# Kernel tuning notes

Hardware: AMD Instinct MI355X
Metric: run time of the kernel (lower is better)

The kernel has to match this reference:

```python
import jax, jax.numpy as jnp
import numpy as np


def _ln(x, g, b, eps=1e-5):
    m = x.mean(-1, keepdims=True)
    v = ((x - m) ** 2).mean(-1, keepdims=True)
    return (x - m) * jax.lax.rsqrt(v + eps) * g + b


def setup_inputs() -> dict:
    key = jax.random.key(0)
    ks = jax.random.split(key, 16)
    B, C, D, H, W = 1, 192, 8, 32, 32
    nh, k, hid = 6, 7, 768
    n = lambda i, shape: jax.random.normal(ks[i], shape, dtype=jnp.float32) * 0.02
    return {
        'x': jax.random.normal(ks[0], (B, C, D, H, W), dtype=jnp.float32),
        'pos_emb': n(1, (1, D, C)),
        't_ln1_g': jnp.ones((C,), jnp.float32), 't_ln1_b': jnp.zeros((C,), jnp.float32),
        't_qkv_w': n(2, (C, 3 * C)),
        't_out_w': n(3, (C, C)), 't_out_b': jnp.zeros((C,), jnp.float32),
        't_ln2_g': jnp.ones((C,), jnp.float32), 't_ln2_b': jnp.zeros((C,), jnp.float32),
        't_fc1_w': n(4, (C, hid)), 't_fc1_b': jnp.zeros((hid,), jnp.float32),
        't_fc2_w': n(5, (hid, C)), 't_fc2_b': jnp.zeros((C,), jnp.float32),
        't_lnf_g': jnp.ones((C,), jnp.float32), 't_lnf_b': jnp.zeros((C,), jnp.float32),
        's_ln1_g': jnp.ones((C,), jnp.float32), 's_ln1_b': jnp.zeros((C,), jnp.float32),
        's_qkv_w': n(6, (C, 3 * C)), 's_qkv_b': jnp.zeros((3 * C,), jnp.float32),
        's_rpb': n(7, (nh, 2 * k - 1, 2 * k - 1)),
        's_proj_w': n(8, (C, C)), 's_proj_b': jnp.zeros((C,), jnp.float32),
        's_ln2_g': jnp.ones((C,), jnp.float32), 's_ln2_b': jnp.zeros((C,), jnp.float32),
        's_fc1_w': n(9, (C, hid)), 's_fc1_b': jnp.zeros((hid,), jnp.float32),
        's_fc2_w': n(10, (hid, C)), 's_fc2_b': jnp.zeros((C,), jnp.float32),
    }


def reference(x, pos_emb, t_ln1_g, t_ln1_b, t_qkv_w, t_out_w, t_out_b,
              t_ln2_g, t_ln2_b, t_fc1_w, t_fc1_b, t_fc2_w, t_fc2_b,
              t_lnf_g, t_lnf_b, s_ln1_g, s_ln1_b, s_qkv_w, s_qkv_b, s_rpb,
              s_proj_w, s_proj_b, s_ln2_g, s_ln2_b, s_fc1_w, s_fc1_b,
              s_fc2_w, s_fc2_b):
    B, C, D, H, W = x.shape
    nh = 6
    d = C // nh
    k = 7
    scale = d ** -0.5

    # ---- Time transformer: attend over the D frames per spatial position ----
    t = jnp.transpose(x, (0, 3, 4, 2, 1)).reshape(B * H * W, D, C)  # (b h w) s c
    t = t + pos_emb
    y = _ln(t, t_ln1_g, t_ln1_b)
    qkv = (y @ t_qkv_w).reshape(-1, D, 3, nh, d)
    q, kk, v = [jnp.transpose(qkv[:, :, i], (0, 2, 1, 3)) for i in range(3)]  # [N,nh,D,d]
    att = jax.nn.softmax(jnp.einsum('nhid,nhjd->nhij', q, kk) * scale, axis=-1)
    o = jnp.einsum('nhij,nhjd->nhid', att, v)
    o = jnp.transpose(o, (0, 2, 1, 3)).reshape(-1, D, C)
    t = t + (o @ t_out_w + t_out_b)
    y = _ln(t, t_ln2_g, t_ln2_b)
    t = t + (jax.nn.gelu(y @ t_fc1_w + t_fc1_b, approximate=False) @ t_fc2_w + t_fc2_b)
    t = _ln(t, t_lnf_g, t_lnf_b)
    x = x + jnp.transpose(t.reshape(B, H, W, D, C), (0, 4, 3, 1, 2))

    # ---- Space transformer: neighborhood (NAT) attention per frame ----
    s = jnp.transpose(x, (0, 2, 3, 4, 1)).reshape(B * D, H, W, C)  # (b s) h w c
    shortcut = s
    y = _ln(s, s_ln1_g, s_ln1_b)
    qkv = (y @ s_qkv_w + s_qkv_b).reshape(B * D, H, W, 3, nh, d)
    qkv = jnp.transpose(qkv, (3, 0, 4, 1, 2, 5))  # [3,N,nh,H,W,d]
    q, kk, v = qkv[0] * scale, qkv[1], qkv[2]
    half = k // 2
    sh = jnp.clip(jnp.arange(H) - half, 0, H - k)   # window start per row (edge-clamped)
    sw = jnp.clip(jnp.arange(W) - half, 0, W - k)
    idx_h = sh[:, None] + jnp.arange(k)             # [H,k] neighbor rows
    idx_w = sw[:, None] + jnp.arange(k)             # [W,k] neighbor cols
    rel_h = idx_h - jnp.arange(H)[:, None] + (k - 1)  # rel-pos-bias indices in [0,2k-2]
    rel_w = idx_w - jnp.arange(W)[:, None] + (k - 1)
    Kn = kk[:, :, idx_h][:, :, :, :, idx_w]  # [N,nh,H,k,W,k,d]
    Vn = v[:, :, idx_h][:, :, :, :, idx_w]
    att = jnp.einsum('nehwd,nehawbd->nehwab', q, Kn)  # [N,nh,H,W,k,k]
    bias = jnp.transpose(s_rpb[:, rel_h][:, :, :, rel_w], (0, 1, 3, 2, 4))  # [nh,H,W,k,k]
    att = att + bias[None]
    shp = att.shape
    att = jax.nn.softmax(att.reshape(shp[0], shp[1], shp[2], shp[3], k * k), axis=-1).reshape(shp)
    o = jnp.einsum('nehwab,nehawbd->nehwd', att, Vn)
    o = jnp.transpose(o, (0, 2, 3, 1, 4)).reshape(B * D, H, W, C)
    s = shortcut + (o @ s_proj_w + s_proj_b)
    y = _ln(s, s_ln2_g, s_ln2_b)
    s = s + (jax.nn.gelu(y @ s_fc1_w + s_fc1_b, approximate=False) @ s_fc2_w + s_fc2_b)
    x_space = jnp.transpose(s.reshape(B, D, H, W, C), (0, 4, 1, 2, 3))
    return x + x_space
```

## Files before the change

kernel.cpp:

```cpp
#include <hip/hip_runtime.h>
#include <hip/hip_bf16.h>
#include <math.h>

typedef __hip_bfloat16 bf16;
typedef short bf16x8 __attribute__((ext_vector_type(8)));
typedef float f32x4 __attribute__((ext_vector_type(4)));

__device__ __forceinline__ float b2f(bf16 v) { return __bfloat162float(v); }
__device__ __forceinline__ bf16 f2b(float v) { return __float2bfloat16(v); }
__device__ __forceinline__ float us2f(unsigned short u) {
  return __uint_as_float(((unsigned)u) << 16);
}
__device__ __forceinline__ unsigned short f2us(float f) {
  bf16 h = __float2bfloat16(f);
  return *reinterpret_cast<unsigned short*>(&h);
}
__device__ __forceinline__ float ldin(const void* p, size_t i, int f32) {
  return f32 ? ((const float*)p)[i] : b2f(((const bf16*)p)[i]);
}

#define CC 192
#define DD 8
#define HH 32
#define WW 32
#define NHEAD 6
#define HDIM 32
#define HID 768
#define NTOK 8192
#define ATT_SCALE 0.17677669529663687f

__global__ void wconv_kernel(const unsigned short* __restrict__ xu,
                             const void* w0, const void* w1, const void* w2,
                             const void* w3, const void* w4, const void* w5,
                             const void* w6, const void* w7,
                             bf16* __restrict__ WT, int* __restrict__ flag) {
  __shared__ int cnt[4];
  {
    float a = fabsf(us2f(xu[threadIdx.x]));
    bool insane = !((a == 0.0f) || (a > 9.5e-7f && a < 64.0f));
    unsigned long long mask = __ballot(insane);
    if ((threadIdx.x & 63) == 0) cnt[threadIdx.x >> 6] = __popcll(mask);
  }
  __syncthreads();
  int f32 = (cnt[0] + cnt[1] + cnt[2] + cnt[3]) > 32;
  if (blockIdx.x == 0 && threadIdx.x == 0) *flag = f32;

  int idx = blockIdx.x * 256 + threadIdx.x;
  if (idx >= 884736) return;
  const void* src; int K, N, loc;
  if      (idx < 110592) { src = w0; K = 192; N = 576; loc = idx; }
  else if (idx < 147456) { src = w1; K = 192; N = 192; loc = idx - 110592; }
  else if (idx < 294912) { src = w2; K = 192; N = 768; loc = idx - 147456; }
  else if (idx < 442368) { src = w3; K = 768; N = 192; loc = idx - 294912; }
  else if (idx < 552960) { src = w4; K = 192; N = 576; loc = idx - 442368; }
  else if (idx < 589824) { src = w5; K = 192; N = 192; loc = idx - 552960; }
  else if (idx < 737280) { src = w6; K = 192; N = 768; loc = idx - 589824; }
  else                   { src = w7; K = 768; N = 192; loc = idx - 737280; }
  int n = loc / K, k = loc - n * K;
  WT[idx] = f2b(ldin(src, (size_t)k * N + n, f32));
}

#define WOFF_TQKV  0
#define WOFF_TOUT  110592
#define WOFF_TFC1  147456
#define WOFF_TFC2  294912
#define WOFF_SQKV  442368
#define WOFF_SPROJ 552960
#define WOFF_SFC1  589824
#define WOFF_SFC2  737280

__global__ void build_ln1_kernel(const void* __restrict__ x, const void* __restrict__ pos,
                                 const void* __restrict__ g, const void* __restrict__ b,
                                 float* __restrict__ T, bf16* __restrict__ Y,
                                 const int* __restrict__ dfl) {
  int f32 = *dfl;
  int wave = (blockIdx.x * blockDim.x + threadIdx.x) >> 6;
  int lane = threadIdx.x & 63;
  if (wave >= NTOK) return;
  int d = wave & 7, hw = wave >> 3;
  float v[3];
#pragma unroll
  for (int e = 0; e < 3; e++) {
    int c = lane + e * 64;
    v[e] = ldin(x, (size_t)((c << 3) + d) * 1024 + hw, f32) +
           ldin(pos, (size_t)d * CC + c, f32);
  }
  float* tr = T + (size_t)wave * CC;
#pragma unroll
  for (int e = 0; e < 3; e++) tr[lane + e * 64] = v[e];
  float s = v[0] + v[1] + v[2];
  for (int off = 32; off; off >>= 1) s += __shfl_xor(s, off);
  float mean = s * (1.0f / CC);
  float d0 = v[0] - mean, d1 = v[1] - mean, d2 = v[2] - mean;
  float q = d0 * d0 + d1 * d1 + d2 * d2;
  for (int off = 32; off; off >>= 1) q += __shfl_xor(q, off);
  float rstd = rsqrtf(q * (1.0f / CC) + 1e-5f);
  bf16* o = Y + (size_t)wave * CC;
  o[lane]       = f2b(d0 * rstd * ldin(g, lane, f32)       + ldin(b, lane, f32));
  o[lane + 64]  = f2b(d1 * rstd * ldin(g, lane + 64, f32)  + ldin(b, lane + 64, f32));
  o[lane + 128] = f2b(d2 * rstd * ldin(g, lane + 128, f32) + ldin(b, lane + 128, f32));
}

__global__ void ln_kernel(const float* __restrict__ in, bf16* __restrict__ out,
                          const void* __restrict__ g, const void* __restrict__ b,
                          int rows, const int* __restrict__ dfl) {
  int f32 = *dfl;
  int wave = (blockIdx.x * blockDim.x + threadIdx.x) >> 6;
  int lane = threadIdx.x & 63;
  if (wave >= rows) return;
  const float* r = in + (size_t)wave * CC;
  float v0 = r[lane], v1 = r[lane + 64], v2 = r[lane + 128];
  float s = v0 + v1 + v2;
  for (int off = 32; off; off >>= 1) s += __shfl_xor(s, off);
  float mean = s * (1.0f / CC);
  float d0 = v0 - mean, d1 = v1 - mean, d2 = v2 - mean;
  float q = d0 * d0 + d1 * d1 + d2 * d2;
  for (int off = 32; off; off >>= 1) q += __shfl_xor(q, off);
  float rstd = rsqrtf(q * (1.0f / CC) + 1e-5f);
  bf16* o = out + (size_t)wave * CC;
  o[lane]       = f2b(d0 * rstd * ldin(g, lane, f32)       + ldin(b, lane, f32));
  o[lane + 64]  = f2b(d1 * rstd * ldin(g, lane + 64, f32)  + ldin(b, lane + 64, f32));
  o[lane + 128] = f2b(d2 * rstd * ldin(g, lane + 128, f32) + ldin(b, lane + 128, f32));
}

template <int TM, bool BIAS, bool GELU, bool RES, bool OUTBF, bool FINAL>
__global__ void gemm_kernel(const bf16* __restrict__ A, const bf16* __restrict__ WT,
                            const void* __restrict__ bias, const float* __restrict__ R,
                            void* __restrict__ Cout, const float* __restrict__ X2,
                            int M, int N, int K, const int* __restrict__ dfl) {
  int f32 = *dfl;
  __shared__ __align__(16) unsigned short As[TM * 64 * 72];
  __shared__ __align__(16) unsigned short Bs[64 * 72];
  int bm = blockIdx.y * (TM * 64), bn = blockIdx.x * 64;
  int tid = threadIdx.x;
  int w = tid >> 6;
  int lane = tid & 63;
  int lm = lane & 15;
  int lk = lane >> 4;

  f32x4 acc[TM][4];
#pragma unroll
  for (int i = 0; i < TM; i++)
#pragma unroll
    for (int j = 0; j < 4; j++) acc[i][j] = (f32x4){0.f, 0.f, 0.f, 0.f};

  const unsigned short* Au = reinterpret_cast<const unsigned short*>(A);
  const unsigned short* Wu = reinterpret_cast<const unsigned short*>(WT);

  for (int k0 = 0; k0 < K; k0 += 64) {
#pragma unroll
    for (int u = 0; u < TM * 2; u++) {
      int unit = tid + u * 256;
      int row = unit >> 3, seg = unit & 7;
      uint4 v = *reinterpret_cast<const uint4*>(
          &Au[(size_t)(bm + row) * K + k0 + seg * 8]);
      *reinterpret_cast<uint4*>(&As[row * 72 + seg * 8]) = v;
    }
#pragma unroll
    for (int u = 0; u < 2; u++) {
      int unit = tid + u * 256;
      int n = unit >> 3, seg = unit & 7;
      uint4 v = *reinterpret_cast<const uint4*>(
          &Wu[(size_t)(bn + n) * K + k0 + seg * 8]);
      *reinterpret_cast<uint4*>(&Bs[n * 72 + seg * 8]) = v;
    }
    __syncthreads();

#pragma unroll
    for (int kc = 0; kc < 2; kc++) {
      bf16x8 af[TM], bfr[4];
#pragma unroll
      for (int tm = 0; tm < TM; tm++)
        af[tm] = *reinterpret_cast<const bf16x8*>(
            &As[(w * (TM * 16) + tm * 16 + lm) * 72 + kc * 32 + lk * 8]);
#pragma unroll
      for (int tn = 0; tn < 4; tn++)
        bfr[tn] = *reinterpret_cast<const bf16x8*>(
            &Bs[(tn * 16 + lm) * 72 + kc * 32 + lk * 8]);
#pragma unroll
      for (int tm = 0; tm < TM; tm++)
#pragma unroll
        for (int tn = 0; tn < 4; tn++)
          acc[tm][tn] = __builtin_amdgcn_mfma_f32_16x16x32_bf16(
              af[tm], bfr[tn], acc[tm][tn], 0, 0, 0);
    }
    __syncthreads();
  }

#pragma unroll
  for (int tn = 0; tn < 4; tn++) {
    int col = bn + tn * 16 + lm;
    float bv = BIAS ? ldin(bias, col, f32) : 0.f;
#pragma unroll
    for (int tm = 0; tm < TM; tm++) {
      int row0 = bm + w * (TM * 16) + tm * 16 + lk * 4;
#pragma unroll
      for (int r = 0; r < 4; r++) {
        int row = row0 + r;
        float v = acc[tm][tn][r];
        if (BIAS) v += bv;
        if (GELU) v = 0.5f * v * (1.0f + erff(v * 0.70710678118654752f));
        size_t idx = (size_t)row * N + col;
        if (RES) v += R[idx];
        if (FINAL) {
          float o = v + X2[(size_t)row * CC + col];
          if (f32) ((float*)Cout)[(size_t)col * NTOK + row] = o;
          else     ((bf16*)Cout)[(size_t)col * NTOK + row] = f2b(o);
        } else if (OUTBF) {
          ((bf16*)Cout)[idx] = f2b(v);
        } else {
          ((float*)Cout)[idx] = v;
        }
      }
    }
  }
}

__global__ void time_attn_kernel(const bf16* __restrict__ qkv, bf16* __restrict__ O) {
  __shared__ float q[NHEAD][DD][HDIM];
  __shared__ float k[NHEAD][DD][HDIM];
  __shared__ float v[NHEAD][DD][HDIM];
  __shared__ float p[NHEAD][DD][DD];
  int n = blockIdx.x;
  int head = threadIdx.x >> 5;
  int dd = threadIdx.x & 31;
  for (int s = 0; s < DD; s++) {
    const bf16* row = qkv + (size_t)(n * DD + s) * (3 * CC);
    q[head][s][dd] = b2f(row[head * HDIM + dd]);
    k[head][s][dd] = b2f(row[CC + head * HDIM + dd]);
    v[head][s][dd] = b2f(row[2 * CC + head * HDIM + dd]);
  }
  __syncthreads();
  for (int pair = dd; pair < 64; pair += 32) {
    int sq = pair >> 3, sk = pair & 7;
    float sum = 0.f;
#pragma unroll
    for (int e = 0; e < HDIM; e++) sum += q[head][sq][e] * k[head][sk][e];
    p[head][sq][sk] = sum * ATT_SCALE;
  }
  __syncthreads();
  if (dd < DD) {
    float mx = -1e30f;
    for (int sk = 0; sk < DD; sk++) mx = fmaxf(mx, p[head][dd][sk]);
    float sum = 0.f;
    for (int sk = 0; sk < DD; sk++) { float e = expf(p[head][dd][sk] - mx); p[head][dd][sk] = e; sum += e; }
    float inv = 1.0f / sum;
    for (int sk = 0; sk < DD; sk++) p[head][dd][sk] *= inv;
  }
  __syncthreads();
  for (int sq = 0; sq < DD; sq++) {
    float sum = 0.f;
#pragma unroll
    for (int sk = 0; sk < DD; sk++) sum += p[head][sq][sk] * v[head][sk][dd];
    O[(size_t)(n * DD + sq) * CC + head * HDIM + dd] = f2b(sum);
  }
}

__global__ void epi_ln1_kernel(const float* __restrict__ T, const void* __restrict__ x,
                               const void* __restrict__ gf, const void* __restrict__ bf,
                               const void* __restrict__ g1, const void* __restrict__ b1,
                               float* __restrict__ X1T, bf16* __restrict__ Y,
                               const int* __restrict__ dfl) {
  int f32 = *dfl;
  int wave = (blockIdx.x * blockDim.x + threadIdx.x) >> 6;
  int lane = threadIdx.x & 63;
  if (wave >= NTOK) return;
  const float* r = T + (size_t)wave * CC;
  float v0 = r[lane], v1 = r[lane + 64], v2 = r[lane + 128];
  float s = v0 + v1 + v2;
  for (int off = 32; off; off >>= 1) s += __shfl_xor(s, off);
  float mean = s * (1.0f / CC);
  float d0 = v0 - mean, d1 = v1 - mean, d2 = v2 - mean;
  float q = d0 * d0 + d1 * d1 + d2 * d2;
  for (int off = 32; off; off >>= 1) q += __shfl_xor(q, off);
  float rstd = rsqrtf(q * (1.0f / CC) + 1e-5f);
  int d = wave & 7, hw = wave >> 3;
  int m = d * 1024 + hw;
  float xv[3];
#pragma unroll
  for (int e = 0; e < 3; e++) {
    int c = lane + e * 64;
    float dv = (e == 0 ? d0 : (e == 1 ? d1 : d2));
    float normed = dv * rstd * ldin(gf, c, f32) + ldin(bf, c, f32);
    xv[e] = ldin(x, (size_t)((c << 3) + d) * 1024 + hw, f32) + normed;
  }
  float* o = X1T + (size_t)m * CC;
#pragma unroll
  for (int e = 0; e < 3; e++) o[lane + e * 64] = xv[e];
  float s2 = xv[0] + xv[1] + xv[2];
  for (int off = 32; off; off >>= 1) s2 += __shfl_xor(s2, off);
  float mean2 = s2 * (1.0f / CC);
  float e0 = xv[0] - mean2, e1 = xv[1] - mean2, e2 = xv[2] - mean2;
  float q2 = e0 * e0 + e1 * e1 + e2 * e2;
  for (int off = 32; off; off >>= 1) q2 += __shfl_xor(q2, off);
  float rstd2 = rsqrtf(q2 * (1.0f / CC) + 1e-5f);
  bf16* y = Y + (size_t)m * CC;
  y[lane]       = f2b(e0 * rstd2 * ldin(g1, lane, f32)       + ldin(b1, lane, f32));
  y[lane + 64]  = f2b(e1 * rstd2 * ldin(g1, lane + 64, f32)  + ldin(b1, lane + 64, f32));
  y[lane + 128] = f2b(e2 * rstd2 * ldin(g1, lane + 128, f32) + ldin(b1, lane + 128, f32));
}

#define NKEY 224
#define PKS 40
#define PVS 232
__global__ void nat_attn_kernel(const bf16* __restrict__ qkv, const void* __restrict__ rpb,
                                bf16* __restrict__ O, const int* __restrict__ dfl) {
  int f32 = *dfl;
  __shared__ __align__(16) unsigned short Ks[NKEY * PKS];
  __shared__ __align__(16) unsigned short Vs[32 * PVS];
  __shared__ __align__(16) unsigned short Qs[64 * PKS];
  __shared__ __align__(16) unsigned short Ps[64 * PVS];
  __shared__ float rb[176];

  int blk = blockIdx.x;
  int frame = blk & 7;
  int rest = blk >> 3;
  int h = rest % 6;
  int tile = rest / 6;
  int ty = tile >> 2, tx = tile & 3;
  int base_h = min(max(ty * 8 - 3, 0), HH - 7);
  int base_w = min(max(tx * 8 - 3, 0), WW - 7);

  int tid = threadIdx.x;

  for (int i = tid; i < 169; i += 256) rb[i] = ldin(rpb, (size_t)h * 169 + i, f32);
  for (int u = tid; u < 784; u += 256) {
    int j = u >> 2, seg = u & 3;
    int a = j / 14, bb = j - a * 14;
    int ih = min(base_h + a, HH - 1), iw = min(base_w + bb, WW - 1);
    int mg = frame * 1024 + ih * 32 + iw;
    uint4 v = *reinterpret_cast<const uint4*>(qkv + (size_t)mg * 576 + 192 + h * 32 + seg * 8);
    *reinterpret_cast<uint4*>(&Ks[j * PKS + seg * 8]) = v;
  }
  for (int u = tid; u < 784; u += 256) {
    int j = u >> 2, seg = u & 3;
    int a = j / 14, bb = j - a * 14;
    int ih = min(base_h + a, HH - 1), iw = min(base_w + bb, WW - 1);
    int mg = frame * 1024 + ih * 32 + iw;
    uint4 v = *reinterpret_cast<const uint4*>(qkv + (size_t)mg * 576 + 384 + h * 32 + seg * 8);
    unsigned arr[4] = {v.x, v.y, v.z, v.w};
#pragma unroll
    for (int e = 0; e < 4; e++) {
      Vs[(seg * 8 + e * 2) * PVS + j]     = (unsigned short)(arr[e] & 0xffffu);
      Vs[(seg * 8 + e * 2 + 1) * PVS + j] = (unsigned short)(arr[e] >> 16);
    }
  }
  for (int u = tid; u < 32 * (PVS - 196); u += 256) {
    int dd = u / (PVS - 196), c = 196 + u % (PVS - 196);
    Vs[dd * PVS + c] = 0;
  }
  {
    int q = tid >> 2, seg = tid & 3;
    int qy = ty * 8 + (q >> 3), qx = tx * 8 + (q & 7);
    int mg = frame * 1024 + qy * 32 + qx;
    uint4 v = *reinterpret_cast<const uint4*>(qkv + (size_t)mg * 576 + h * 32 + seg * 8);
    *reinterpret_cast<uint4*>(&Qs[q * PKS + seg * 8]) = v;
  }
  __syncthreads();

  int w = tid >> 6;
  int lane = tid & 63;
  int c = lane & 15;
  int lk = lane >> 4;

  bf16x8 aq = *reinterpret_cast<const bf16x8*>(&Qs[(w * 16 + c) * PKS + lk * 8]);
  f32x4 sc[14];
#pragma unroll
  for (int f = 0; f < 14; f++) {
    bf16x8 bk = *reinterpret_cast<const bf16x8*>(&Ks[(f * 16 + c) * PKS + lk * 8]);
    sc[f] = __builtin_amdgcn_mfma_f32_16x16x32_bf16(aq, bk, (f32x4){0.f, 0.f, 0.f, 0.f}, 0, 0, 0);
  }

#pragma unroll
  for (int f = 0; f < 14; f++) {
    int key = f * 16 + c;
    int a = key / 14, bb = key - a * 14;
    int ih = base_h + a, iw = base_w + bb;
    bool keyok = key < 196;
#pragma unroll
    for (int r = 0; r < 4; r++) {
      int qloc = w * 16 + lk * 4 + r;
      int qy = ty * 8 + (qloc >> 3), qx = tx * 8 + (qloc & 7);
      int sh = min(max(qy - 3, 0), HH - 7);
      int sw = min(max(qx - 3, 0), WW - 7);
      bool valid = keyok && ((unsigned)(ih - sh) < 7u) && ((unsigned)(iw - sw) < 7u);
      int bidx = valid ? (ih - qy + 6) * 13 + (iw - qx + 6) : 0;
      float s = sc[f][r] * ATT_SCALE + rb[bidx];
      sc[f][r] = valid ? s : -1e30f;
    }
  }

  float sm[4];
#pragma unroll
  for (int r = 0; r < 4; r++) {
    float m = sc[0][r];
#pragma unroll
    for (int f = 1; f < 14; f++) m = fmaxf(m, sc[f][r]);
    for (int off = 8; off; off >>= 1) m = fmaxf(m, __shfl_xor(m, off));
    float s = 0.f;
#pragma unroll
    for (int f = 0; f < 14; f++) { float e = __expf(sc[f][r] - m); sc[f][r] = e; s += e; }
    for (int off = 8; off; off >>= 1) s += __shfl_xor(s, off);
    sm[r] = 1.0f / s;
  }
#pragma unroll
  for (int f = 0; f < 14; f++)
#pragma unroll
    for (int r = 0; r < 4; r++)
      Ps[(w * 16 + lk * 4 + r) * PVS + f * 16 + c] = f2us(sc[f][r] * sm[r]);
  __syncthreads();

  f32x4 oacc[2] = {(f32x4){0.f, 0.f, 0.f, 0.f}, (f32x4){0.f, 0.f, 0.f, 0.f}};
#pragma unroll
  for (int kt = 0; kt < 7; kt++) {
    bf16x8 ap = *reinterpret_cast<const bf16x8*>(&Ps[(w * 16 + c) * PVS + kt * 32 + lk * 8]);
#pragma unroll
    for (int dt = 0; dt < 2; dt++) {
      bf16x8 bv = *reinterpret_cast<const bf16x8*>(&Vs[(dt * 16 + c) * PVS + kt * 32 + lk * 8]);
      oacc[dt] = __builtin_amdgcn_mfma_f32_16x16x32_bf16(ap, bv, oacc[dt], 0, 0, 0);
    }
  }

#pragma unroll
  for (int dt = 0; dt < 2; dt++)
#pragma unroll
    for (int r = 0; r < 4; r++) {
      int qloc = w * 16 + lk * 4 + r;
      int qy = ty * 8 + (qloc >> 3), qx = tx * 8 + (qloc & 7);
      int mg = frame * 1024 + qy * 32 + qx;
      O[(size_t)mg * CC + h * 32 + dt * 16 + c] = f2b(oacc[dt][r]);
    }
}

extern "C" void kernel_launch(void* const* d_in, const int* in_sizes, int n_in,
                              void* d_out, int out_size, void* d_ws, size_t ws_size,
                              hipStream_t stream) {
  const void* x        = d_in[0];
  const void* pos_emb  = d_in[1];
  const void* t_ln1_g  = d_in[2];
  const void* t_ln1_b  = d_in[3];
  const void* t_qkv_w  = d_in[4];
  const void* t_out_w  = d_in[5];
  const void* t_out_b  = d_in[6];
  const void* t_ln2_g  = d_in[7];
  const void* t_ln2_b  = d_in[8];
  const void* t_fc1_w  = d_in[9];
  const void* t_fc1_b  = d_in[10];
  const void* t_fc2_w  = d_in[11];
  const void* t_fc2_b  = d_in[12];
  const void* t_lnf_g  = d_in[13];
  const void* t_lnf_b  = d_in[14];
  const void* s_ln1_g  = d_in[15];
  const void* s_ln1_b  = d_in[16];
  const void* s_qkv_w  = d_in[17];
  const void* s_qkv_b  = d_in[18];
  const void* s_rpb    = d_in[19];
  const void* s_proj_w = d_in[20];
  const void* s_proj_b = d_in[21];
  const void* s_ln2_g  = d_in[22];
  const void* s_ln2_b  = d_in[23];
  const void* s_fc1_w  = d_in[24];
  const void* s_fc1_b  = d_in[25];
  const void* s_fc2_w  = d_in[26];
  const void* s_fc2_b  = d_in[27];

  float* ws = (float*)d_ws;
  const size_t SZ = (size_t)NTOK * CC;
  const size_t need = (5 * SZ + 4 + 442368 + 16) * sizeof(float);
  if (ws_size < need) return;

  float* T   = ws;
  float* X1T = ws + SZ;
  bf16*  Y   = (bf16*)(ws + 2 * SZ);
  bf16*  O   = (bf16*)(ws + 2 * SZ + SZ / 2);
  bf16*  QKV = (bf16*)(ws + 3 * SZ);
  bf16*  Hb  = QKV;
  float* S   = T;
  int*   dfl = (int*)(ws + 5 * SZ);
  bf16*  WT  = (bf16*)(ws + 5 * SZ + 4);

  dim3 blk256(256);

  wconv_kernel<<<3456, blk256, 0, stream>>>(
      (const unsigned short*)x,
      t_qkv_w, t_out_w, t_fc1_w, t_fc2_w, s_qkv_w, s_proj_w, s_fc1_w, s_fc2_w, WT, dfl);

  build_ln1_kernel<<<NTOK / 4, blk256, 0, stream>>>(x, pos_emb, t_ln1_g, t_ln1_b, T, Y, dfl);
  gemm_kernel<2, false, false, false, true, false><<<dim3(9, 64), blk256, 0, stream>>>(
      Y, WT + WOFF_TQKV, nullptr, nullptr, QKV, nullptr, NTOK, 3 * CC, CC, dfl);
  time_attn_kernel<<<1024, 192, 0, stream>>>(QKV, O);
  gemm_kernel<1, true, false, true, false, false><<<dim3(3, 128), blk256, 0, stream>>>(
      O, WT + WOFF_TOUT, t_out_b, T, T, nullptr, NTOK, CC, CC, dfl);
  ln_kernel<<<NTOK / 4, blk256, 0, stream>>>(T, Y, t_ln2_g, t_ln2_b, NTOK, dfl);
  gemm_kernel<2, true, true, false, true, false><<<dim3(12, 64), blk256, 0, stream>>>(
      Y, WT + WOFF_TFC1, t_fc1_b, nullptr, Hb, nullptr, NTOK, HID, CC, dfl);
  gemm_kernel<1, true, false, true, false, false><<<dim3(3, 128), blk256, 0, stream>>>(
      Hb, WT + WOFF_TFC2, t_fc2_b, T, T, nullptr, NTOK, CC, HID, dfl);
  epi_ln1_kernel<<<NTOK / 4, blk256, 0, stream>>>(
      T, x, t_lnf_g, t_lnf_b, s_ln1_g, s_ln1_b, X1T, Y, dfl);

  gemm_kernel<2, true, false, false, true, false><<<dim3(9, 64), blk256, 0, stream>>>(
      Y, WT + WOFF_SQKV, s_qkv_b, nullptr, QKV, nullptr, NTOK, 3 * CC, CC, dfl);
  nat_attn_kernel<<<768, blk256, 0, stream>>>(QKV, s_rpb, O, dfl);
  gemm_kernel<1, true, false, true, false, false><<<dim3(3, 128), blk256, 0, stream>>>(
      O, WT + WOFF_SPROJ, s_proj_b, X1T, S, nullptr, NTOK, CC, CC, dfl);
  ln_kernel<<<NTOK / 4, blk256, 0, stream>>>(S, Y, s_ln2_g, s_ln2_b, NTOK, dfl);
  gemm_kernel<2, true, true, false, true, false><<<dim3(12, 64), blk256, 0, stream>>>(
      Y, WT + WOFF_SFC1, s_fc1_b, nullptr, Hb, nullptr, NTOK, HID, CC, dfl);
  gemm_kernel<1, true, false, true, false, true><<<dim3(3, 128), blk256, 0, stream>>>(
      Hb, WT + WOFF_SFC2, s_fc2_b, S, d_out, X1T, NTOK, CC, HID, dfl);
}
```

Baseline: 274.2 us.

## Fuse all stages into a cooperative persistent megakernel with grid syncs

```diff
diff --git a/kernel.cpp b/kernel.cpp
--- a/kernel.cpp
+++ b/kernel.cpp
@@ -1,6 +1,9 @@
 #include <hip/hip_runtime.h>
 #include <hip/hip_bf16.h>
+#include <hip/hip_cooperative_groups.h>
 #include <math.h>
+
+namespace cg = cooperative_groups;
 
 typedef __hip_bfloat16 bf16;
 typedef short bf16x8 __attribute__((ext_vector_type(8)));
@@ -29,37 +32,6 @@
 #define NTOK 8192
 #define ATT_SCALE 0.17677669529663687f
 
-__global__ void wconv_kernel(const unsigned short* __restrict__ xu,
-                             const void* w0, const void* w1, const void* w2,
-                             const void* w3, const void* w4, const void* w5,
-                             const void* w6, const void* w7,
-                             bf16* __restrict__ WT, int* __restrict__ flag) {
-  __shared__ int cnt[4];
-  {
-    float a = fabsf(us2f(xu[threadIdx.x]));
-    bool insane = !((a == 0.0f) || (a > 9.5e-7f && a < 64.0f));
-    unsigned long long mask = __ballot(insane);
-    if ((threadIdx.x & 63) == 0) cnt[threadIdx.x >> 6] = __popcll(mask);
-  }
-  __syncthreads();
-  int f32 = (cnt[0] + cnt[1] + cnt[2] + cnt[3]) > 32;
-  if (blockIdx.x == 0 && threadIdx.x == 0) *flag = f32;
-
-  int idx = blockIdx.x * 256 + threadIdx.x;
-  if (idx >= 884736) return;
-  const void* src; int K, N, loc;
-  if      (idx < 110592) { src = w0; K = 192; N = 576; loc = idx; }
-  else if (idx < 147456) { src = w1; K = 192; N = 192; loc = idx - 110592; }
-  else if (idx < 294912) { src = w2; K = 192; N = 768; loc = idx - 147456; }
-  else if (idx < 442368) { src = w3; K = 768; N = 192; loc = idx - 294912; }
-  else if (idx < 552960) { src = w4; K = 192; N = 576; loc = idx - 442368; }
-  else if (idx < 589824) { src = w5; K = 192; N = 192; loc = idx - 552960; }
-  else if (idx < 737280) { src = w6; K = 192; N = 768; loc = idx - 589824; }
-  else                   { src = w7; K = 768; N = 192; loc = idx - 737280; }
-  int n = loc / K, k = loc - n * K;
-  WT[idx] = f2b(ldin(src, (size_t)k * N + n, f32));
-}
-
 #define WOFF_TQKV  0
 #define WOFF_TOUT  110592
 #define WOFF_TFC1  147456
@@ -69,444 +41,589 @@
 #define WOFF_SFC1  589824
 #define WOFF_SFC2  737280
 
-__global__ void build_ln1_kernel(const void* __restrict__ x, const void* __restrict__ pos,
-                                 const void* __restrict__ g, const void* __restrict__ b,
-                                 float* __restrict__ T, bf16* __restrict__ Y,
-                                 const int* __restrict__ dfl) {
-  int f32 = *dfl;
-  int wave = (blockIdx.x * blockDim.x + threadIdx.x) >> 6;
-  int lane = threadIdx.x & 63;
-  if (wave >= NTOK) return;
-  int d = wave & 7, hw = wave >> 3;
-  float v[3];
-#pragma unroll
-  for (int e = 0; e < 3; e++) {
-    int c = lane + e * 64;
-    v[e] = ldin(x, (size_t)((c << 3) + d) * 1024 + hw, f32) +
-           ldin(pos, (size_t)d * CC + c, f32);
-  }
-  float* tr = T + (size_t)wave * CC;
-#pragma unroll
-  for (int e = 0; e < 3; e++) tr[lane + e * 64] = v[e];
-  float s = v[0] + v[1] + v[2];
-  for (int off = 32; off; off >>= 1) s += __shfl_xor(s, off);
-  float mean = s * (1.0f / CC);
-  float d0 = v[0] - mean, d1 = v[1] - mean, d2 = v[2] - mean;
-  float q = d0 * d0 + d1 * d1 + d2 * d2;
-  for (int off = 32; off; off >>= 1) q += __shfl_xor(q, off);
-  float rstd = rsqrtf(q * (1.0f / CC) + 1e-5f);
-  bf16* o = Y + (size_t)wave * CC;
-  o[lane]       = f2b(d0 * rstd * ldin(g, lane, f32)       + ldin(b, lane, f32));
-  o[lane + 64]  = f2b(d1 * rstd * ldin(g, lane + 64, f32)  + ldin(b, lane + 64, f32));
-  o[lane + 128] = f2b(d2 * rstd * ldin(g, lane + 128, f32) + ldin(b, lane + 128, f32));
-}
-
-__global__ void ln_kernel(const float* __restrict__ in, bf16* __restrict__ out,
-                          const void* __restrict__ g, const void* __restrict__ b,
-                          int rows, const int* __restrict__ dfl) {
-  int f32 = *dfl;
-  int wave = (blockIdx.x * blockDim.x + threadIdx.x) >> 6;
-  int lane = threadIdx.x & 63;
-  if (wave >= rows) return;
-  const float* r = in + (size_t)wave * CC;
-  float v0 = r[lane], v1 = r[lane + 64], v2 = r[lane + 128];
-  float s = v0 + v1 + v2;
-  for (int off = 32; off; off >>= 1) s += __shfl_xor(s, off);
-  float mean = s * (1.0f / CC);
-  float d0 = v0 - mean, d1 = v1 - mean, d2 = v2 - mean;
-  float q = d0 * d0 + d1 * d1 + d2 * d2;
-  for (int off = 32; off; off >>= 1) q += __shfl_xor(q, off);
-  float rstd = rsqrtf(q * (1.0f / CC) + 1e-5f);
-  bf16* o = out + (size_t)wave * CC;
-  o[lane]       = f2b(d0 * rstd * ldin(g, lane, f32)       + ldin(b, lane, f32));
-  o[lane + 64]  = f2b(d1 * rstd * ldin(g, lane + 64, f32)  + ldin(b, lane + 64, f32));
-  o[lane + 128] = f2b(d2 * rstd * ldin(g, lane + 128, f32) + ldin(b, lane + 128, f32));
+#define PKS 40
+#define PVS 232
+struct SmemGemm {
+  unsigned short As[128 * 72];
+  unsigned short Bs[64 * 72];
+};
+struct SmemNat {
+  unsigned short Ks[224 * PKS];
+  unsigned short Vs[32 * PVS];
+  unsigned short Qs[64 * PKS];
+  unsigned short Ps[64 * PVS];
+  float rb[176];
+};
+struct SmemTA {
+  float q[NHEAD][DD][HDIM];
+  float k[NHEAD][DD][HDIM];
+  float v[NHEAD][DD][HDIM];
+  float p[NHEAD][DD][DD];
+};
+union Smem {
+  SmemGemm g;
+  SmemNat n;
+  SmemTA t;
+};
+
+struct KArgs {
+  const void *x, *pos;
+  const void *t_ln1_g, *t_ln1_b, *t_out_b, *t_ln2_g, *t_ln2_b;
+  const void *t_fc1_b, *t_fc2_b, *t_lnf_g, *t_lnf_b;
+  const void *s_ln1_g, *s_ln1_b, *s_qkv_b, *s_rpb, *s_proj_b;
+  const void *s_ln2_g, *s_ln2_b, *s_fc1_b, *s_fc2_b;
+  const void *w0, *w1, *w2, *w3, *w4, *w5, *w6, *w7;
+  void* out;
+  float* T; float* X1T; bf16* Y; bf16* O; bf16* QKV; bf16* WT;
+};
+
+__device__ void st_wconv(const KArgs& a, int f32) {
+  for (int idx = blockIdx.x * 256 + threadIdx.x; idx < 884736; idx += gridDim.x * 256) {
+    const void* src; int K, N, loc;
+    if      (idx < 110592) { src = a.w0; K = 192; N = 576; loc = idx; }
+    else if (idx < 147456) { src = a.w1; K = 192; N = 192; loc = idx - 110592; }
+    else if (idx < 294912) { src = a.w2; K = 192; N = 768; loc = idx - 147456; }
+    else if (idx < 442368) { src = a.w3; K = 768; N = 192; loc = idx - 294912; }
+    else if (idx < 552960) { src = a.w4; K = 192; N = 576; loc = idx - 442368; }
+    else if (idx < 589824) { src = a.w5; K = 192; N = 192; loc = idx - 552960; }
+    else if (idx < 737280) { src = a.w6; K = 192; N = 768; loc = idx - 589824; }
+    else                   { src = a.w7; K = 768; N = 192; loc = idx - 737280; }
+    int n = loc / K, k = loc - n * K;
+    a.WT[idx] = f2b(ldin(src, (size_t)k * N + n, f32));
+  }
+}
+
+__device__ void st_build_ln1(const KArgs& a, int f32) {
+  int w = threadIdx.x >> 6, lane = threadIdx.x & 63;
+  for (int row = blockIdx.x * 4 + w; row < NTOK; row += gridDim.x * 4) {
+    int d = row & 7, hw = row >> 3;
+    float v[3];
+#pragma unroll
+    for (int e = 0; e < 3; e++) {
+      int c = lane + e * 64;
+      v[e] = ldin(a.x, (size_t)((c << 3) + d) * 1024 + hw, f32) +
+             ldin(a.pos, (size_t)d * CC + c, f32);
+    }
+    float* tr = a.T + (size_t)row * CC;
+#pragma unroll
+    for (int e = 0; e < 3; e++) tr[lane + e * 64] = v[e];
+    float s = v[0] + v[1] + v[2];
+    for (int off = 32; off; off >>= 1) s += __shfl_xor(s, off);
+    float mean = s * (1.0f / CC);
+    float d0 = v[0] - mean, d1 = v[1] - mean, d2 = v[2] - mean;
+    float q = d0 * d0 + d1 * d1 + d2 * d2;
+    for (int off = 32; off; off >>= 1) q += __shfl_xor(q, off);
+    float rstd = rsqrtf(q * (1.0f / CC) + 1e-5f);
+    bf16* o = a.Y + (size_t)row * CC;
+    o[lane]       = f2b(d0 * rstd * ldin(a.t_ln1_g, lane, f32)       + ldin(a.t_ln1_b, lane, f32));
+    o[lane + 64]  = f2b(d1 * rstd * ldin(a.t_ln1_g, lane + 64, f32)  + ldin(a.t_ln1_b, lane + 64, f32));
+    o[lane + 128] = f2b(d2 * rstd * ldin(a.t_ln1_g, lane + 128, f32) + ldin(a.t_ln1_b, lane + 128, f32));
+  }
+}
+
+__device__ void st_ln(const float* in, bf16* out, const void* g, const void* b, int f32) {
+  int w = threadIdx.x >> 6, lane = threadIdx.x & 63;
+  for (int row = blockIdx.x * 4 + w; row < NTOK; row += gridDim.x * 4) {
+    const float* r = in + (size_t)row * CC;
+    float v0 = r[lane], v1 = r[lane + 64], v2 = r[lane + 128];
+    float s = v0 + v1 + v2;
+    for (int off = 32; off; off >>= 1) s += __shfl_xor(s, off);
+    float mean = s * (1.0f / CC);
+    float d0 = v0 - mean, d1 = v1 - mean, d2 = v2 - mean;
+    float q = d0 * d0 + d1 * d1 + d2 * d2;
+    for (int off = 32; off; off >>= 1) q += __shfl_xor(q, off);
+    float rstd = rsqrtf(q * (1.0f / CC) + 1e-5f);
+    bf16* o = out + (size_t)row * CC;
+    o[lane]       = f2b(d0 * rstd * ldin(g, lane, f32)       + ldin(b, lane, f32));
+    o[lane + 64]  = f2b(d1 * rstd * ldin(g, lane + 64, f32)  + ldin(b, lane + 64, f32));
+    o[lane + 128] = f2b(d2 * rstd * ldin(g, lane + 128, f32) + ldin(b, lane + 128, f32));
+  }
+}
+
+__device__ void st_epi_ln1(const KArgs& a, int f32) {
+  int w = threadIdx.x >> 6, lane = threadIdx.x & 63;
+  for (int row = blockIdx.x * 4 + w; row < NTOK; row += gridDim.x * 4) {
+    const float* r = a.T + (size_t)row * CC;
+    float v0 = r[lane], v1 = r[lane + 64], v2 = r[lane + 128];
+    float s = v0 + v1 + v2;
+    for (int off = 32; off; off >>= 1) s += __shfl_xor(s, off);
+    float mean = s * (1.0f / CC);
+    float d0 = v0 - mean, d1 = v1 - mean, d2 = v2 - mean;
+    float q = d0 * d0 + d1 * d1 + d2 * d2;
+    for (int off = 32; off; off >>= 1) q += __shfl_xor(q, off);
+    float rstd = rsqrtf(q * (1.0f / CC) + 1e-5f);
+    int d = row & 7, hw = row >> 3;
+    int m = d * 1024 + hw;
+    float xv[3];
+#pragma unroll
+    for (int e = 0; e < 3; e++) {
+      int c = lane + e * 64;
+      float dv = (e == 0 ? d0 : (e == 1 ? d1 : d2));
+      float normed = dv * rstd * ldin(a.t_lnf_g, c, f32) + ldin(a.t_lnf_b, c, f32);
+      xv[e] = ldin(a.x, (size_t)((c << 3) + d) * 1024 + hw, f32) + normed;
+    }
+    float* o = a.X1T + (size_t)m * CC;
+#pragma unroll
+    for (int e = 0; e < 3; e++) o[lane + e * 64] = xv[e];
+    float s2 = xv[0] + xv[1] + xv[2];
+    for (int off = 32; off; off >>= 1) s2 += __shfl_xor(s2, off);
+    float mean2 = s2 * (1.0f / CC);
+    float e0 = xv[0] - mean2, e1 = xv[1] - mean2, e2 = xv[2] - mean2;
+    float q2 = e0 * e0 + e1 * e1 + e2 * e2;
+    for (int off = 32; off; off >>= 1) q2 += __shfl_xor(q2, off);
+    float rstd2 = rsqrtf(q2 * (1.0f / CC) + 1e-5f);
+    bf16* y = a.Y + (size_t)m * CC;
+    y[lane]       = f2b(e0 * rstd2 * ldin(a.s_ln1_g, lane, f32)       + ldin(a.s_ln1_b, lane, f32));
+    y[lane + 64]  = f2b(e1 * rstd2 * ldin(a.s_ln1_g, lane + 64, f32)  + ldin(a.s_ln1_b, lane + 64, f32));
+    y[lane + 128] = f2b(e2 * rstd2 * ldin(a.s_ln1_g, lane + 128, f32) + ldin(a.s_ln1_b, lane + 128, f32));
+  }
 }
 
 template <int TM, bool BIAS, bool GELU, bool RES, bool OUTBF, bool FINAL>
-__global__ void gemm_kernel(const bf16* __restrict__ A, const bf16* __restrict__ WT,
-                            const void* __restrict__ bias, const float* __restrict__ R,
-                            void* __restrict__ Cout, const float* __restrict__ X2,
-                            int M, int N, int K, const int* __restrict__ dfl) {
-  int f32 = *dfl;
-  __shared__ __align__(16) unsigned short As[TM * 64 * 72];
-  __shared__ __align__(16) unsigned short Bs[64 * 72];
-  int bm = blockIdx.y * (TM * 64), bn = blockIdx.x * 64;
+__device__ void st_gemm(SmemGemm& sm, const bf16* A, const bf16* WT,
+                        const void* bias, const float* R, void* Cout,
+                        const float* X2, int N, int K, int nbx, int f32) {
   int tid = threadIdx.x;
-  int w = tid >> 6;
-  int lane = tid & 63;
-  int lm = lane & 15;
-  int lk = lane >> 4;
-
-  f32x4 acc[TM][4];
-#pragma unroll
-  for (int i = 0; i < TM; i++)
-#pragma unroll
-    for (int j = 0; j < 4; j++) acc[i][j] = (f32x4){0.f, 0.f, 0.f, 0.f};
-
+  int w = tid >> 6, lane = tid & 63, lm = lane & 15, lk = lane >> 4;
   const unsigned short* Au = reinterpret_cast<const unsigned short*>(A);
   const unsigned short* Wu = reinterpret_cast<const unsigned short*>(WT);
-
-  for (int k0 = 0; k0 < K; k0 += 64) {
-#pragma unroll
-    for (int u = 0; u < TM * 2; u++) {
-      int unit = tid + u * 256;
-      int row = unit >> 3, seg = unit & 7;
-      uint4 v = *reinterpret_cast<const uint4*>(
-          &Au[(size_t)(bm + row) * K + k0 + seg * 8]);
-      *reinterpret_cast<uint4*>(&As[row * 72 + seg * 8]) = v;
-    }
-#pragma unroll
-    for (int u = 0; u < 2; u++) {
-      int unit = tid + u * 256;
-      int n = unit >> 3, seg = unit & 7;
-      uint4 v = *reinterpret_cast<const uint4*>(
-          &Wu[(size_t)(bn + n) * K + k0 + seg * 8]);
-      *reinterpret_cast<uint4*>(&Bs[n * 72 + seg * 8]) = v;
-    }
-    __syncthreads();
-
-#pragma unroll
-    for (int kc = 0; kc < 2; kc++) {
-      bf16x8 af[TM], bfr[4];
-#pragma unroll
-      for (int tm = 0; tm < TM; tm++)
-        af[tm] = *reinterpret_cast<const bf16x8*>(
-            &As[(w * (TM * 16) + tm * 16 + lm) * 72 + kc * 32 + lk * 8]);
-#pragma unroll
-      for (int tn = 0; tn < 4; tn++)
-        bfr[tn] = *reinterpret_cast<const bf16x8*>(
-            &Bs[(tn * 16 + lm) * 72 + kc * 32 + lk * 8]);
-#pragma unroll
-      for (int tm = 0; tm < TM; tm++)
+  int njobs = nbx * (NTOK / (TM * 64));
+  for (int job = blockIdx.x; job < njobs; job += gridDim.x) {
+    __syncthreads();
+    int bxk = job % nbx, byk = job / nbx;
+    int bm = byk * (TM * 64), bn = bxk * 64;
+    f32x4 acc[TM][4];
+#pragma unroll
+    for (int i = 0; i < TM; i++)
+#pragma unroll
+      for (int j = 0; j < 4; j++) acc[i][j] = (f32x4){0.f, 0.f, 0.f, 0.f};
+
+    for (int k0 = 0; k0 < K; k0 += 64) {
+#pragma unroll
+      for (int u = 0; u < TM * 2; u++) {
+        int unit = tid + u * 256;
+        int row = unit >> 3, seg = unit & 7;
+        uint4 v = *reinterpret_cast<const uint4*>(
+            &Au[(size_t)(bm + row) * K + k0 + seg * 8]);
+        *reinterpret_cast<uint4*>(&sm.As[row * 72 + seg * 8]) = v;
+      }
+#pragma unroll
+      for (int u = 0; u < 2; u++) {
+        int unit = tid + u * 256;
+        int n = unit >> 3, seg = unit & 7;
+        uint4 v = *reinterpret_cast<const uint4*>(
+            &Wu[(size_t)(bn + n) * K + k0 + seg * 8]);
+        *reinterpret_cast<uint4*>(&sm.Bs[n * 72 + seg * 8]) = v;
+      }
+      __syncthreads();
+#pragma unroll
+      for (int kc = 0; kc < 2; kc++) {
+        bf16x8 af[TM], bfr[4];
+#pragma unroll
+        for (int tm = 0; tm < TM; tm++)
+          af[tm] = *reinterpret_cast<const bf16x8*>(
+              &sm.As[(w * (TM * 16) + tm * 16 + lm) * 72 + kc * 32 + lk * 8]);
 #pragma unroll
         for (int tn = 0; tn < 4; tn++)
-          acc[tm][tn] = __builtin_amdgcn_mfma_f32_16x16x32_bf16(
-              af[tm], bfr[tn], acc[tm][tn], 0, 0, 0);
-    }
-    __syncthreads();
-  }
-
-#pragma unroll
-  for (int tn = 0; tn < 4; tn++) {
-    int col = bn + tn * 16 + lm;
-    float bv = BIAS ? ldin(bias, col, f32) : 0.f;
-#pragma unroll
-    for (int tm = 0; tm < TM; tm++) {
-      int row0 = bm + w * (TM * 16) + tm * 16 + lk * 4;
-#pragma unroll
-      for (int r = 0; r < 4; r++) {
-        int row = row0 + r;
-        float v = acc[tm][tn][r];
-        if (BIAS) v += bv;
-        if (GELU) v = 0.5f * v * (1.0f + erff(v * 0.70710678118654752f));
-        size_t idx = (size_t)row * N + col;
-        if (RES) v += R[idx];
-        if (FINAL) {
-          float o = v + X2[(size_t)row * CC + col];
-          if (f32) ((float*)Cout)[(size_t)col * NTOK + row] = o;
-          else     ((bf16*)Cout)[(size_t)col * NTOK + row] = f2b(o);
-        } else if (OUTBF) {
-          ((bf16*)Cout)[idx] = f2b(v);
-        } else {
-          ((float*)Cout)[idx] = v;
+          bfr[tn] = *reinterpret_cast<const bf16x8*>(
+              &sm.Bs[(tn * 16 + lm) * 72 + kc * 32 + lk * 8]);
+#pragma unroll
+        for (int tm = 0; tm < TM; tm++)
+#pragma unroll
+          for (int tn = 0; tn < 4; tn++)
+            acc[tm][tn] = __builtin_amdgcn_mfma_f32_16x16x32_bf16(
+                af[tm], bfr[tn], acc[tm][tn], 0, 0, 0);
+      }
+      __syncthreads();
+    }
+
+#pragma unroll
+    for (int tn = 0; tn < 4; tn++) {
+      int col = bn + tn * 16 + lm;
+      float bv = BIAS ? ldin(bias, col, f32) : 0.f;
+#pragma unroll
+      for (int tm = 0; tm < TM; tm++) {
+        int row0 = bm + w * (TM * 16) + tm * 16 + lk * 4;
+#pragma unroll
+        for (int r = 0; r < 4; r++) {
+          int row = row0 + r;
+          float v = acc[tm][tn][r];
+          if (BIAS) v += bv;
+          if (GELU) v = 0.5f * v * (1.0f + erff(v * 0.70710678118654752f));
+          size_t idx = (size_t)row * N + col;
+          if (RES) v += R[idx];
+          if (FINAL) {
+            float o = v + X2[(size_t)row * CC + col];
+            if (f32) ((float*)Cout)[(size_t)col * NTOK + row] = o;
+            else     ((bf16*)Cout)[(size_t)col * NTOK + row] = f2b(o);
+          } else if (OUTBF) {
+            ((bf16*)Cout)[idx] = f2b(v);
+          } else {
+            ((float*)Cout)[idx] = v;
+          }
         }
       }
     }
   }
 }
 
-__global__ void time_attn_kernel(const bf16* __restrict__ qkv, bf16* __restrict__ O) {
-  __shared__ float q[NHEAD][DD][HDIM];
-  __shared__ float k[NHEAD][DD][HDIM];
-  __shared__ float v[NHEAD][DD][HDIM];
-  __shared__ float p[NHEAD][DD][DD];
-  int n = blockIdx.x;
+__device__ void st_time_attn(SmemTA& sm, const bf16* qkv, bf16* O) {
+  bool act = threadIdx.x < 192;
   int head = threadIdx.x >> 5;
   int dd = threadIdx.x & 31;
-  for (int s = 0; s < DD; s++) {
-    const bf16* row = qkv + (size_t)(n * DD + s) * (3 * CC);
-    q[head][s][dd] = b2f(row[head * HDIM + dd]);
-    k[head][s][dd] = b2f(row[CC + head * HDIM + dd]);
-    v[head][s][dd] = b2f(row[2 * CC + head * HDIM + dd]);
+  for (int n = blockIdx.x; n < 1024; n += gridDim.x) {
+    __syncthreads();
+    if (act) {
+      for (int s = 0; s < DD; s++) {
+        const bf16* row = qkv + (size_t)(n * DD + s) * (3 * CC);
+        sm.q[head][s][dd] = b2f(row[head * HDIM + dd]);
+        sm.k[head][s][dd] = b2f(row[CC + head * HDIM + dd]);
+        sm.v[head][s][dd] = b2f(row[2 * CC + head * HDIM + dd]);
+      }
+    }
+    __syncthreads();
+    if (act) {
+      for (int pair = dd; pair < 64; pair += 32) {
+        int sq = pair >> 3, sk = pair & 7;
+        float sum = 0.f;
+#pragma unroll
+        for (int e = 0; e < HDIM; e++) sum += sm.q[head][sq][e] * sm.k[head][sk][e];
+        sm.p[head][sq][sk] = sum * ATT_SCALE;
+      }
+    }
+    __syncthreads();
+    if (act && dd < DD) {
+      float mx = -1e30f;
+      for (int sk = 0; sk < DD; sk++) mx = fmaxf(mx, sm.p[head][dd][sk]);
+      float sum = 0.f;
+      for (int sk = 0; sk < DD; sk++) { float e = expf(sm.p[head][dd][sk] - mx); sm.p[head][dd][sk] = e; sum += e; }
+      float inv = 1.0f / sum;
+      for (int sk = 0; sk < DD; sk++) sm.p[head][dd][sk] *= inv;
+    }
+    __syncthreads();
+    if (act) {
+      for (int sq = 0; sq < DD; sq++) {
+        float sum = 0.f;
+#pragma unroll
+        for (int sk = 0; sk < DD; sk++) sum += sm.p[head][sq][sk] * sm.v[head][sk][dd];
+        O[(size_t)(n * DD + sq) * CC + head * HDIM + dd] = f2b(sum);
+      }
+    }
+  }
+}
+
+__device__ void st_nat(SmemNat& sm, const bf16* qkv, const void* rpb, bf16* O, int f32) {
+  int tid = threadIdx.x;
+  for (int job = blockIdx.x; job < 768; job += gridDim.x) {
+    __syncthreads();
+    int frame = job & 7;
+    int rest = job >> 3;
+    int h = rest % 6;
+    int tile = rest / 6;
+    int ty = tile >> 2, tx = tile & 3;
+    int base_h = min(max(ty * 8 - 3, 0), HH - 7);
+    int base_w = min(max(tx * 8 - 3, 0), WW - 7);
+
+    for (int i = tid; i < 169; i += 256) sm.rb[i] = ldin(rpb, (size_t)h * 169 + i, f32);
+    for (int u = tid; u < 784; u += 256) {
+      int j = u >> 2, seg = u & 3;
+      int a2 = j / 14, bb = j - a2 * 14;
+      int ih = min(base_h + a2, HH - 1), iw = min(base_w + bb, WW - 1);
+      int mg = frame * 1024 + ih * 32 + iw;
+      uint4 v = *reinterpret_cast<const uint4*>(qkv + (size_t)mg * 576 + 192 + h * 32 + seg * 8);
+      *reinterpret_cast<uint4*>(&sm.Ks[j * PKS + seg * 8]) = v;
+    }
+    for (int u = tid; u < 784; u += 256) {
+      int j = u >> 2, seg = u & 3;
+      int a2 = j / 14, bb = j - a2 * 14;
+      int ih = min(base_h + a2, HH - 1), iw = min(base_w + bb, WW - 1);
+      int mg = frame * 1024 + ih * 32 + iw;
+      uint4 v = *reinterpret_cast<const uint4*>(qkv + (size_t)mg * 576 + 384 + h * 32 + seg * 8);
+      unsigned arr[4] = {v.x, v.y, v.z, v.w};
+#pragma unroll
+      for (int e = 0; e < 4; e++) {
+        sm.Vs[(seg * 8 + e * 2) * PVS + j]     = (unsigned short)(arr[e] & 0xffffu);
+        sm.Vs[(seg * 8 + e * 2 + 1) * PVS + j] = (unsigned short)(arr[e] >> 16);
+      }
+    }
+    for (int u = tid; u < 32 * (PVS - 196); u += 256) {
+      int dd = u / (PVS - 196), c2 = 196 + u % (PVS - 196);
+      sm.Vs[dd * PVS + c2] = 0;
+    }
+    {
+      int q = tid >> 2, seg = tid & 3;
+      int qy = ty * 8 + (q >> 3), qx = tx * 8 + (q & 7);
+      int mg = frame * 1024 + qy * 32 + qx;
+      uint4 v = *reinterpret_cast<const uint4*>(qkv + (size_t)mg * 576 + h * 32 + seg * 8);
+      *reinterpret_cast<uint4*>(&sm.Qs[q * PKS + seg * 8]) = v;
+    }
+    __syncthreads();
+
+    int w = tid >> 6;
+    int lane = tid & 63;
+    int c = lane & 15;
+    int lk = lane >> 4;
+
+    bf16x8 aq = *reinterpret_cast<const bf16x8*>(&sm.Qs[(w * 16 + c) * PKS + lk * 8]);
+    f32x4 sc[14];
+#pragma unroll
+    for (int f = 0; f < 14; f++) {
+      bf16x8 bk = *reinterpret_cast<const bf16x8*>(&sm.Ks[(f * 16 + c) * PKS + lk * 8]);
+      sc[f] = __builtin_amdgcn_mfma_f32_16x16x32_bf16(aq, bk, (f32x4){0.f, 0.f, 0.f, 0.f}, 0, 0, 0);
+    }
+
+#pragma unroll
+    for (int f = 0; f < 14; f++) {
+      int key = f * 16 + c;
+      int a2 = key / 14, bb = key - a2 * 14;
+      int ih = base_h + a2, iw = base_w + bb;
+      bool keyok = key < 196;
+#pragma unroll
+      for (int r = 0; r < 4; r++) {
+        int qloc = w * 16 + lk * 4 + r;
+        int qy = ty * 8 + (qloc >> 3), qx = tx * 8 + (qloc & 7);
+        int sh = min(max(qy - 3, 0), HH - 7);
+        int sw = min(max(qx - 3, 0), WW - 7);
+        bool valid = keyok && ((unsigned)(ih - sh) < 7u) && ((unsigned)(iw - sw) < 7u);
+        int bidx = valid ? (ih - qy + 6) * 13 + (iw - qx + 6) : 0;
+        float s = sc[f][r] * ATT_SCALE + sm.rb[bidx];
+        sc[f][r] = valid ? s : -1e30f;
+      }
+    }
+
+    float smx[4];
+#pragma unroll
+    for (int r = 0; r < 4; r++) {
+      float m = sc[0][r];
+#pragma unroll
+      for (int f = 1; f < 14; f++) m = fmaxf(m, sc[f][r]);
+      for (int off = 8; off; off >>= 1) m = fmaxf(m, __shfl_xor(m, off));
+      float s = 0.f;
+#pragma unroll
+      for (int f = 0; f < 14; f++) { float e = __expf(sc[f][r] - m); sc[f][r] = e; s += e; }
+      for (int off = 8; off; off >>= 1) s += __shfl_xor(s, off);
+      smx[r] = 1.0f / s;
+    }
+#pragma unroll
+    for (int f = 0; f < 14; f++)
+#pragma unroll
+      for (int r = 0; r < 4; r++)
+        sm.Ps[(w * 16 + lk * 4 + r) * PVS + f * 16 + c] = f2us(sc[f][r] * smx[r]);
+    __syncthreads();
+
+    f32x4 oacc[2] = {(f32x4){0.f, 0.f, 0.f, 0.f}, (f32x4){0.f, 0.f, 0.f, 0.f}};
+#pragma unroll
+    for (int kt = 0; kt < 7; kt++) {
+      bf16x8 ap = *reinterpret_cast<const bf16x8*>(&sm.Ps[(w * 16 + c) * PVS + kt * 32 + lk * 8]);
+#pragma unroll
+      for (int dt = 0; dt < 2; dt++) {
+        bf16x8 bv = *reinterpret_cast<const bf16x8*>(&sm.Vs[(dt * 16 + c) * PVS + kt * 32 + lk * 8]);
+        oacc[dt] = __builtin_amdgcn_mfma_f32_16x16x32_bf16(ap, bv, oacc[dt], 0, 0, 0);
+      }
+    }
+#pragma unroll
+    for (int dt = 0; dt < 2; dt++)
+#pragma unroll
+      for (int r = 0; r < 4; r++) {
+        int qloc = w * 16 + lk * 4 + r;
+        int qy = ty * 8 + (qloc >> 3), qx = tx * 8 + (qloc & 7);
+        int mg = frame * 1024 + qy * 32 + qx;
+        O[(size_t)mg * CC + h * 32 + dt * 16 + c] = f2b(oacc[dt][r]);
+      }
+  }
+}
+
+__global__ void __launch_bounds__(256, 2) mega_kernel(KArgs a) {
+  __shared__ __align__(16) Smem sm;
+  __shared__ int cnt[4];
+  int f32;
+  {
+    float v = fabsf(us2f(((const unsigned short*)a.x)[threadIdx.x]));
+    bool insane = !((v == 0.0f) || (v > 9.5e-7f && v < 64.0f));
+    unsigned long long m = __ballot(insane);
+    if ((threadIdx.x & 63) == 0) cnt[threadIdx.x >> 6] = __popcll(m);
   }
   __syncthreads();
-  for (int pair = dd; pair < 64; pair += 32) {
-    int sq = pair >> 3, sk = pair & 7;
-    float sum = 0.f;
-#pragma unroll
-    for (int e = 0; e < HDIM; e++) sum += q[head][sq][e] * k[head][sk][e];
-    p[head][sq][sk] = sum * ATT_SCALE;
-  }
+  f32 = (cnt[0] + cnt[1] + cnt[2] + cnt[3]) > 32;
+
+  cg::grid_group grid = cg::this_grid();
+
+  st_wconv(a, f32);                                       grid.sync();
+  st_build_ln1(a, f32);                                   grid.sync();
+  st_gemm<2, false, false, false, true, false>(sm.g, a.Y, a.WT + WOFF_TQKV,
+      nullptr, nullptr, a.QKV, nullptr, 3 * CC, CC, 9, f32);      grid.sync();
+  st_time_attn(sm.t, a.QKV, a.O);                         grid.sync();
+  st_gemm<1, true, false, true, false, false>(sm.g, a.O, a.WT + WOFF_TOUT,
+      a.t_out_b, a.T, a.T, nullptr, CC, CC, 3, f32);              grid.sync();
+  st_ln(a.T, a.Y, a.t_ln2_g, a.t_ln2_b, f32);             grid.sync();
+  st_gemm<2, true, true, false, true, false>(sm.g, a.Y, a.WT + WOFF_TFC1,
+      a.t_fc1_b, nullptr, a.QKV , nullptr, HID, CC, 12, f32); grid.sync();
+  st_gemm<1, true, false, true, false, false>(sm.g, a.QKV , a.WT + WOFF_TFC2,
+      a.t_fc2_b, a.T, a.T, nullptr, CC, HID, 3, f32);             grid.sync();
+  st_epi_ln1(a, f32);                                     grid.sync();
+  st_gemm<2, true, false, false, true, false>(sm.g, a.Y, a.WT + WOFF_SQKV,
+      a.s_qkv_b, nullptr, a.QKV, nullptr, 3 * CC, CC, 9, f32);    grid.sync();
+  st_nat(sm.n, a.QKV, a.s_rpb, a.O, f32);                 grid.sync();
+  st_gemm<1, true, false, true, false, false>(sm.g, a.O, a.WT + WOFF_SPROJ,
+      a.s_proj_b, a.X1T, a.T, nullptr, CC, CC, 3, f32);           grid.sync();
+  st_ln(a.T, a.Y, a.s_ln2_g, a.s_ln2_b, f32);             grid.sync();
+  st_gemm<2, true, true, false, true, false>(sm.g, a.Y, a.WT + WOFF_SFC1,
+      a.s_fc1_b, nullptr, a.QKV , nullptr, HID, CC, 12, f32); grid.sync();
+  st_gemm<1, true, false, true, false, true>(sm.g, a.QKV , a.WT + WOFF_SFC2,
+      a.s_fc2_b, a.T, a.out, a.X1T, CC, HID, 3, f32);
+}
+
+__device__ int probe_local(const unsigned short* xu) {
+  __shared__ int cnt[4];
+  float v = fabsf(us2f(xu[threadIdx.x]));
+  bool insane = !((v == 0.0f) || (v > 9.5e-7f && v < 64.0f));
+  unsigned long long m = __ballot(insane);
+  if ((threadIdx.x & 63) == 0) cnt[threadIdx.x >> 6] = __popcll(m);
   __syncthreads();
-  if (dd < DD) {
-    float mx = -1e30f;
-    for (int sk = 0; sk < DD; sk++) mx = fmaxf(mx, p[head][dd][sk]);
-    float sum = 0.f;
-    for (int sk = 0; sk < DD; sk++) { float e = expf(p[head][dd][sk] - mx); p[head][dd][sk] = e; sum += e; }
-    float inv = 1.0f / sum;
-    for (int sk = 0; sk < DD; sk++) p[head][dd][sk] *= inv;
-  }
+  int f = (cnt[0] + cnt[1] + cnt[2] + cnt[3]) > 32;
   __syncthreads();
-  for (int sq = 0; sq < DD; sq++) {
-    float sum = 0.f;
-#pragma unroll
-    for (int sk = 0; sk < DD; sk++) sum += p[head][sq][sk] * v[head][sk][dd];
-    O[(size_t)(n * DD + sq) * CC + head * HDIM + dd] = f2b(sum);
-  }
-}
-
-__global__ void epi_ln1_kernel(const float* __restrict__ T, const void* __restrict__ x,
-                               const void* __restrict__ gf, const void* __restrict__ bf,
-                               const void* __restrict__ g1, const void* __restrict__ b1,
-                               float* __restrict__ X1T, bf16* __restrict__ Y,
-                               const int* __restrict__ dfl) {
-  int f32 = *dfl;
-  int wave = (blockIdx.x * blockDim.x + threadIdx.x) >> 6;
-  int lane = threadIdx.x & 63;
-  if (wave >= NTOK) return;
-  const float* r = T + (size_t)wave * CC;
-  float v0 = r[lane], v1 = r[lane + 64], v2 = r[lane + 128];
-  float s = v0 + v1 + v2;
-  for (int off = 32; off; off >>= 1) s += __shfl_xor(s, off);
-  float mean = s * (1.0f / CC);
-  float d0 = v0 - mean, d1 = v1 - mean, d2 = v2 - mean;
-  float q = d0 * d0 + d1 * d1 + d2 * d2;
-  for (int off = 32; off; off >>= 1) q += __shfl_xor(q, off);
-  float rstd = rsqrtf(q * (1.0f / CC) + 1e-5f);
-  int d = wave & 7, hw = wave >> 3;
-  int m = d * 1024 + hw;
-  float xv[3];
-#pragma unroll
-  for (int e = 0; e < 3; e++) {
-    int c = lane + e * 64;
-    float dv = (e == 0 ? d0 : (e == 1 ? d1 : d2));
-    float normed = dv * rstd * ldin(gf, c, f32) + ldin(bf, c, f32);
-    xv[e] = ldin(x, (size_t)((c << 3) + d) * 1024 + hw, f32) + normed;
-  }
-  float* o = X1T + (size_t)m * CC;
-#pragma unroll
-  for (int e = 0; e < 3; e++) o[lane + e * 64] = xv[e];
-  float s2 = xv[0] + xv[1] + xv[2];
-  for (int off = 32; off; off >>= 1) s2 += __shfl_xor(s2, off);
-  float mean2 = s2 * (1.0f / CC);
-  float e0 = xv[0] - mean2, e1 = xv[1] - mean2, e2 = xv[2] - mean2;
-  float q2 = e0 * e0 + e1 * e1 + e2 * e2;
-  for (int off = 32; off; off >>= 1) q2 += __shfl_xor(q2, off);
-  float rstd2 = rsqrtf(q2 * (1.0f / CC) + 1e-5f);
-  bf16* y = Y + (size_t)m * CC;
-  y[lane]       = f2b(e0 * rstd2 * ldin(g1, lane, f32)       + ldin(b1, lane, f32));
-  y[lane + 64]  = f2b(e1 * rstd2 * ldin(g1, lane + 64, f32)  + ldin(b1, lane + 64, f32));
-  y[lane + 128] = f2b(e2 * rstd2 * ldin(g1, lane + 128, f32) + ldin(b1, lane + 128, f32));
-}
-
-#define NKEY 224
-#define PKS 40
-#define PVS 232
-__global__ void nat_attn_kernel(const bf16* __restrict__ qkv, const void* __restrict__ rpb,
-                                bf16* __restrict__ O, const int* __restrict__ dfl) {
-  int f32 = *dfl;
-  __shared__ __align__(16) unsigned short Ks[NKEY * PKS];
-  __shared__ __align__(16) unsigned short Vs[32 * PVS];
-  __shared__ __align__(16) unsigned short Qs[64 * PKS];
-  __shared__ __align__(16) unsigned short Ps[64 * PVS];
-  __shared__ float rb[176];
-
-  int blk = blockIdx.x;
-  int frame = blk & 7;
-  int rest = blk >> 3;
-  int h = rest % 6;
-  int tile = rest / 6;
-  int ty = tile >> 2, tx = tile & 3;
-  int base_h = min(max(ty * 8 - 3, 0), HH - 7);
-  int base_w = min(max(tx * 8 - 3, 0), WW - 7);
-
-  int tid = threadIdx.x;
-
-  for (int i = tid; i < 169; i += 256) rb[i] = ldin(rpb, (size_t)h * 169 + i, f32);
-  for (int u = tid; u < 784; u += 256) {
-    int j = u >> 2, seg = u & 3;
-    int a = j / 14, bb = j - a * 14;
-    int ih = min(base_h + a, HH - 1), iw = min(base_w + bb, WW - 1);
-    int mg = frame * 1024 + ih * 32 + iw;
-    uint4 v = *reinterpret_cast<const uint4*>(qkv + (size_t)mg * 576 + 192 + h * 32 + seg * 8);
-    *reinterpret_cast<uint4*>(&Ks[j * PKS + seg * 8]) = v;
-  }
-  for (int u = tid; u < 784; u += 256) {
-    int j = u >> 2, seg = u & 3;
-    int a = j / 14, bb = j - a * 14;
-    int ih = min(base_h + a, HH - 1), iw = min(base_w + bb, WW - 1);
-    int mg = frame * 1024 + ih * 32 + iw;
-    uint4 v = *reinterpret_cast<const uint4*>(qkv + (size_t)mg * 576 + 384 + h * 32 + seg * 8);
-    unsigned arr[4] = {v.x, v.y, v.z, v.w};
-#pragma unroll
-    for (int e = 0; e < 4; e++) {
-      Vs[(seg * 8 + e * 2) * PVS + j]     = (unsigned short)(arr[e] & 0xffffu);
-      Vs[(seg * 8 + e * 2 + 1) * PVS + j] = (unsigned short)(arr[e] >> 16);
-    }
-  }
-  for (int u = tid; u < 32 * (PVS - 196); u += 256) {
-    int dd = u / (PVS - 196), c = 196 + u % (PVS - 196);
-    Vs[dd * PVS + c] = 0;
-  }
-  {
-    int q = tid >> 2, seg = tid & 3;
-    int qy = ty * 8 + (q >> 3), qx = tx * 8 + (q & 7);
-    int mg = frame * 1024 + qy * 32 + qx;
-    uint4 v = *reinterpret_cast<const uint4*>(qkv + (size_t)mg * 576 + h * 32 + seg * 8);
-    *reinterpret_cast<uint4*>(&Qs[q * PKS + seg * 8]) = v;
-  }
-  __syncthreads();
-
-  int w = tid >> 6;
-  int lane = tid & 63;
-  int c = lane & 15;
-  int lk = lane >> 4;
-
-  bf16x8 aq = *reinterpret_cast<const bf16x8*>(&Qs[(w * 16 + c) * PKS + lk * 8]);
-  f32x4 sc[14];
-#pragma unroll
-  for (int f = 0; f < 14; f++) {
-    bf16x8 bk = *reinterpret_cast<const bf16x8*>(&Ks[(f * 16 + c) * PKS + lk * 8]);
-    sc[f] = __builtin_amdgcn_mfma_f32_16x16x32_bf16(aq, bk, (f32x4){0.f, 0.f, 0.f, 0.f}, 0, 0, 0);
-  }
-
-#pragma unroll
-  for (int f = 0; f < 14; f++) {
-    int key = f * 16 + c;
-    int a = key / 14, bb = key - a * 14;
-    int ih = base_h + a, iw = base_w + bb;
-    bool keyok = key < 196;
-#pragma unroll
-    for (int r = 0; r < 4; r++) {
-      int qloc = w * 16 + lk * 4 + r;
-      int qy = ty * 8 + (qloc >> 3), qx = tx * 8 + (qloc & 7);
-      int sh = min(max(qy - 3, 0), HH - 7);
-      int sw = min(max(qx - 3, 0), WW - 7);
-      bool valid = keyok && ((unsigned)(ih - sh) < 7u) && ((unsigned)(iw - sw) < 7u);
-      int bidx = valid ? (ih - qy + 6) * 13 + (iw - qx + 6) : 0;
-      float s = sc[f][r] * ATT_SCALE + rb[bidx];
-      sc[f][r] = valid ? s : -1e30f;
-    }
-  }
-
-  float sm[4];
-#pragma unroll
-  for (int r = 0; r < 4; r++) {
-    float m = sc[0][r];
-#pragma unroll
-    for (int f = 1; f < 14; f++) m = fmaxf(m, sc[f][r]);
-    for (int off = 8; off; off >>= 1) m = fmaxf(m, __shfl_xor(m, off));
-    float s = 0.f;
-#pragma unroll
-    for (int f = 0; f < 14; f++) { float e = __expf(sc[f][r] - m); sc[f][r] = e; s += e; }
-    for (int off = 8; off; off >>= 1) s += __shfl_xor(s, off);
-    sm[r] = 1.0f / s;
-  }
-#pragma unroll
-  for (int f = 0; f < 14; f++)
-#pragma unroll
-    for (int r = 0; r < 4; r++)
-      Ps[(w * 16 + lk * 4 + r) * PVS + f * 16 + c] = f2us(sc[f][r] * sm[r]);
-  __syncthreads();
-
-  f32x4 oacc[2] = {(f32x4){0.f, 0.f, 0.f, 0.f}, (f32x4){0.f, 0.f, 0.f, 0.f}};
-#pragma unroll
-  for (int kt = 0; kt < 7; kt++) {
-    bf16x8 ap = *reinterpret_cast<const bf16x8*>(&Ps[(w * 16 + c) * PVS + kt * 32 + lk * 8]);
-#pragma unroll
-    for (int dt = 0; dt < 2; dt++) {
-      bf16x8 bv = *reinterpret_cast<const bf16x8*>(&Vs[(dt * 16 + c) * PVS + kt * 32 + lk * 8]);
-      oacc[dt] = __builtin_amdgcn_mfma_f32_16x16x32_bf16(ap, bv, oacc[dt], 0, 0, 0);
-    }
-  }
-
-#pragma unroll
-  for (int dt = 0; dt < 2; dt++)
-#pragma unroll
-    for (int r = 0; r < 4; r++) {
-      int qloc = w * 16 + lk * 4 + r;
-      int qy = ty * 8 + (qloc >> 3), qx = tx * 8 + (qloc & 7);
-      int mg = frame * 1024 + qy * 32 + qx;
-      O[(size_t)mg * CC + h * 32 + dt * 16 + c] = f2b(oacc[dt][r]);
-    }
+  return f;
+}
+__global__ void __launch_bounds__(256, 2) k_wconv(KArgs a) {
+  int f32 = probe_local((const unsigned short*)a.x);
+  st_wconv(a, f32);
+}
+__global__ void __launch_bounds__(256, 2) k_build(KArgs a) {
+  int f32 = probe_local((const unsigned short*)a.x);
+  st_build_ln1(a, f32);
+}
+__global__ void __launch_bounds__(256, 2) k_ln2t(KArgs a) {
+  int f32 = probe_local((const unsigned short*)a.x);
+  st_ln(a.T, a.Y, a.t_ln2_g, a.t_ln2_b, f32);
+}
+__global__ void __launch_bounds__(256, 2) k_ln2s(KArgs a) {
+  int f32 = probe_local((const unsigned short*)a.x);
+  st_ln(a.T, a.Y, a.s_ln2_g, a.s_ln2_b, f32);
+}
+__global__ void __launch_bounds__(256, 2) k_epi(KArgs a) {
+  int f32 = probe_local((const unsigned short*)a.x);
+  st_epi_ln1(a, f32);
+}
+__global__ void __launch_bounds__(256, 2) k_tattn(KArgs a) {
+  __shared__ __align__(16) SmemTA sm;
+  st_time_attn(sm, a.QKV, a.O);
+}
+__global__ void __launch_bounds__(256, 2) k_nat(KArgs a) {
+  __shared__ __align__(16) SmemNat sm;
+  int f32 = probe_local((const unsigned short*)a.x);
+  st_nat(sm, a.QKV, a.s_rpb, a.O, f32);
+}
+__global__ void __launch_bounds__(256, 2) k_g_tqkv(KArgs a) {
+  __shared__ __align__(16) SmemGemm sm;
+  int f32 = probe_local((const unsigned short*)a.x);
+  st_gemm<2, false, false, false, true, false>(sm, a.Y, a.WT + WOFF_TQKV,
+      nullptr, nullptr, a.QKV, nullptr, 3 * CC, CC, 9, f32);
+}
+__global__ void __launch_bounds__(256, 2) k_g_tout(KArgs a) {
+  __shared__ __align__(16) SmemGemm sm;
+  int f32 = probe_local((const unsigned short*)a.x);
+  st_gemm<1, true, false, true, false, false>(sm, a.O, a.WT + WOFF_TOUT,
+      a.t_out_b, a.T, a.T, nullptr, CC, CC, 3, f32);
+}
+__global__ void __launch_bounds__(256, 2) k_g_tfc1(KArgs a) {
+  __shared__ __align__(16) SmemGemm sm;
+  int f32 = probe_local((const unsigned short*)a.x);
+  st_gemm<2, true, true, false, true, false>(sm, a.Y, a.WT + WOFF_TFC1,
+      a.t_fc1_b, nullptr, a.QKV, nullptr, HID, CC, 12, f32);
+}
+__global__ void __launch_bounds__(256, 2) k_g_tfc2(KArgs a) {
+  __shared__ __align__(16) SmemGemm sm;
+  int f32 = probe_local((const unsigned short*)a.x);
+  st_gemm<1, true, false, true, false, false>(sm, a.QKV, a.WT + WOFF_TFC2,
+      a.t_fc2_b, a.T, a.T, nullptr, CC, HID, 3, f32);
+}
+__global__ void __launch_bounds__(256, 2) k_g_sqkv(KArgs a) {
+  __shared__ __align__(16) SmemGemm sm;
+  int f32 = probe_local((const unsigned short*)a.x);
+  st_gemm<2, true, false, false, true, false>(sm, a.Y, a.WT + WOFF_SQKV,
+      a.s_qkv_b, nullptr, a.QKV, nullptr, 3 * CC, CC, 9, f32);
+}
+__global__ void __launch_bounds__(256, 2) k_g_sproj(KArgs a) {
+  __shared__ __align__(16) SmemGemm sm;
+  int f32 = probe_local((const unsigned short*)a.x);
+  st_gemm<1, true, false, true, false, false>(sm, a.O, a.WT + WOFF_SPROJ,
+      a.s_proj_b, a.X1T, a.T, nullptr, CC, CC, 3, f32);
+}
+__global__ void __launch_bounds__(256, 2) k_g_sfc1(KArgs a) {
+  __shared__ __align__(16) SmemGemm sm;
+  int f32 = probe_local((const unsigned short*)a.x);
+  st_gemm<2, true, true, false, true, false>(sm, a.Y, a.WT + WOFF_SFC1,
+      a.s_fc1_b, nullptr, a.QKV, nullptr, HID, CC, 12, f32);
+}
+__global__ void __launch_bounds__(256, 2) k_g_sfc2(KArgs a) {
+  __shared__ __align__(16) SmemGemm sm;
+  int f32 = probe_local((const unsigned short*)a.x);
+  st_gemm<1, true, false, true, false, true>(sm, a.QKV, a.WT + WOFF_SFC2,
+      a.s_fc2_b, a.T, a.out, a.X1T, CC, HID, 3, f32);
 }
 
 extern "C" void kernel_launch(void* const* d_in, const int* in_sizes, int n_in,
                               void* d_out, int out_size, void* d_ws, size_t ws_size,
                               hipStream_t stream) {
-  const void* x        = d_in[0];
-  const void* pos_emb  = d_in[1];
-  const void* t_ln1_g  = d_in[2];
-  const void* t_ln1_b  = d_in[3];
-  const void* t_qkv_w  = d_in[4];
-  const void* t_out_w  = d_in[5];
-  const void* t_out_b  = d_in[6];
-  const void* t_ln2_g  = d_in[7];
-  const void* t_ln2_b  = d_in[8];
-  const void* t_fc1_w  = d_in[9];
-  const void* t_fc1_b  = d_in[10];
-  const void* t_fc2_w  = d_in[11];
-  const void* t_fc2_b  = d_in[12];
-  const void* t_lnf_g  = d_in[13];
-  const void* t_lnf_b  = d_in[14];
-  const void* s_ln1_g  = d_in[15];
-  const void* s_ln1_b  = d_in[16];
-  const void* s_qkv_w  = d_in[17];
-  const void* s_qkv_b  = d_in[18];
-  const void* s_rpb    = d_in[19];
-  const void* s_proj_w = d_in[20];
-  const void* s_proj_b = d_in[21];
-  const void* s_ln2_g  = d_in[22];
-  const void* s_ln2_b  = d_in[23];
-  const void* s_fc1_w  = d_in[24];
-  const void* s_fc1_b  = d_in[25];
-  const void* s_fc2_w  = d_in[26];
-  const void* s_fc2_b  = d_in[27];
-
   float* ws = (float*)d_ws;
   const size_t SZ = (size_t)NTOK * CC;
   const size_t need = (5 * SZ + 4 + 442368 + 16) * sizeof(float);
   if (ws_size < need) return;
 
-  float* T   = ws;
-  float* X1T = ws + SZ;
-  bf16*  Y   = (bf16*)(ws + 2 * SZ);
-  bf16*  O   = (bf16*)(ws + 2 * SZ + SZ / 2);
-  bf16*  QKV = (bf16*)(ws + 3 * SZ);
-  bf16*  Hb  = QKV;
-  float* S   = T;
-  int*   dfl = (int*)(ws + 5 * SZ);
-  bf16*  WT  = (bf16*)(ws + 5 * SZ + 4);
-
-  dim3 blk256(256);
-
-  wconv_kernel<<<3456, blk256, 0, stream>>>(
-      (const unsigned short*)x,
-      t_qkv_w, t_out_w, t_fc1_w, t_fc2_w, s_qkv_w, s_proj_w, s_fc1_w, s_fc2_w, WT, dfl);
-
-  build_ln1_kernel<<<NTOK / 4, blk256, 0, stream>>>(x, pos_emb, t_ln1_g, t_ln1_b, T, Y, dfl);
-  gemm_kernel<2, false, false, false, true, false><<<dim3(9, 64), blk256, 0, stream>>>(
-      Y, WT + WOFF_TQKV, nullptr, nullptr, QKV, nullptr, NTOK, 3 * CC, CC, dfl);
-  time_attn_kernel<<<1024, 192, 0, stream>>>(QKV, O);
-  gemm_kernel<1, true, false, true, false, false><<<dim3(3, 128), blk256, 0, stream>>>(
-      O, WT + WOFF_TOUT, t_out_b, T, T, nullptr, NTOK, CC, CC, dfl);
-  ln_kernel<<<NTOK / 4, blk256, 0, stream>>>(T, Y, t_ln2_g, t_ln2_b, NTOK, dfl);
-  gemm_kernel<2, true, true, false, true, false><<<dim3(12, 64), blk256, 0, stream>>>(
-      Y, WT + WOFF_TFC1, t_fc1_b, nullptr, Hb, nullptr, NTOK, HID, CC, dfl);
-  gemm_kernel<1, true, false, true, false, false><<<dim3(3, 128), blk256, 0, stream>>>(
-      Hb, WT + WOFF_TFC2, t_fc2_b, T, T, nullptr, NTOK, CC, HID, dfl);
-  epi_ln1_kernel<<<NTOK / 4, blk256, 0, stream>>>(
-      T, x, t_lnf_g, t_lnf_b, s_ln1_g, s_ln1_b, X1T, Y, dfl);
-
-  gemm_kernel<2, true, false, false, true, false><<<dim3(9, 64), blk256, 0, stream>>>(
-      Y, WT + WOFF_SQKV, s_qkv_b, nullptr, QKV, nullptr, NTOK, 3 * CC, CC, dfl);
-  nat_attn_kernel<<<768, blk256, 0, stream>>>(QKV, s_rpb, O, dfl);
-  gemm_kernel<1, true, false, true, false, false><<<dim3(3, 128), blk256, 0, stream>>>(
-      O, WT + WOFF_SPROJ, s_proj_b, X1T, S, nullptr, NTOK, CC, CC, dfl);
-  ln_kernel<<<NTOK / 4, blk256, 0, stream>>>(S, Y, s_ln2_g, s_ln2_b, NTOK, dfl);
-  gemm_kernel<2, true, true, false, true, false><<<dim3(12, 64), blk256, 0, stream>>>(
-      Y, WT + WOFF_SFC1, s_fc1_b, nullptr, Hb, nullptr, NTOK, HID, CC, dfl);
-  gemm_kernel<1, true, false, true, false, true><<<dim3(3, 128), blk256, 0, stream>>>(
-      Hb, WT + WOFF_SFC2, s_fc2_b, S, d_out, X1T, NTOK, CC, HID, dfl);
-}
+  KArgs a;
+  a.x       = d_in[0];  a.pos     = d_in[1];
+  a.t_ln1_g = d_in[2];  a.t_ln1_b = d_in[3];
+  a.w0      = d_in[4];
+  a.w1      = d_in[5];  a.t_out_b = d_in[6];
+  a.t_ln2_g = d_in[7];  a.t_ln2_b = d_in[8];
+  a.w2      = d_in[9];  a.t_fc1_b = d_in[10];
+  a.w3      = d_in[11]; a.t_fc2_b = d_in[12];
+  a.t_lnf_g = d_in[13]; a.t_lnf_b = d_in[14];
+  a.s_ln1_g = d_in[15]; a.s_ln1_b = d_in[16];
+  a.w4      = d_in[17]; a.s_qkv_b = d_in[18];
+  a.s_rpb   = d_in[19];
+  a.w5      = d_in[20]; a.s_proj_b = d_in[21];
+  a.s_ln2_g = d_in[22]; a.s_ln2_b = d_in[23];
+  a.w6      = d_in[24]; a.s_fc1_b = d_in[25];
+  a.w7      = d_in[26]; a.s_fc2_b = d_in[27];
+  a.out = d_out;
+  a.T   = ws;
+  a.X1T = ws + SZ;
+  a.Y   = (bf16*)(ws + 2 * SZ);
+  a.O   = (bf16*)(ws + 2 * SZ + SZ / 2);
+  a.QKV = (bf16*)(ws + 3 * SZ);
+  a.WT  = (bf16*)(ws + 5 * SZ + 4);
+
+  int dev = 0, coop = 0;
+  hipGetDevice(&dev);
+  hipDeviceGetAttribute(&coop, hipDeviceAttributeCooperativeLaunch, dev);
+  if (coop) {
+    int maxBlk = 0;
+    if (hipOccupancyMaxActiveBlocksPerMultiprocessor(&maxBlk, mega_kernel, 256, 0)
+            == hipSuccess && maxBlk >= 1) {
+      int gridSz = maxBlk * 256;
+      if (gridSz > 512) gridSz = 512;
+      void* params[] = { (void*)&a };
+      if (hipLaunchCooperativeKernel(mega_kernel, dim3(gridSz), dim3(256),
+                                     params, 0u, stream) == hipSuccess)
+        return;
+    }
+  }
+
+  dim3 blk(256);
+  k_wconv <<<3456, blk, 0, stream>>>(a);
+  k_build <<<512, blk, 0, stream>>>(a);
+  k_g_tqkv<<<576, blk, 0, stream>>>(a);
+  k_tattn <<<512, blk, 0, stream>>>(a);
+  k_g_tout<<<384, blk, 0, stream>>>(a);
+  k_ln2t  <<<512, blk, 0, stream>>>(a);
+  k_g_tfc1<<<768, blk, 0, stream>>>(a);
+  k_g_tfc2<<<384, blk, 0, stream>>>(a);
+  k_epi   <<<512, blk, 0, stream>>>(a);
+  k_g_sqkv<<<576, blk, 0, stream>>>(a);
+  k_nat   <<<768, blk, 0, stream>>>(a);
+  k_g_sproj<<<384, blk, 0, stream>>>(a);
+  k_ln2s  <<<512, blk, 0, stream>>>(a);
+  k_g_sfc1<<<768, blk, 0, stream>>>(a);
+  k_g_sfc2<<<384, blk, 0, stream>>>(a);
+}
```

New measurement: 839.8 us. 206% more time.
